# Kernel optimization log

Hardware: AMD Instinct MI355X
Metric: run time of the kernel (lower is better)

The kernel has to match this reference:

```python
import jax, jax.numpy as jnp
import numpy as np

D = 256; H = 8; L = 4; K = 4; AS = 2; HD = D // H
KK = K * K
LEVEL_SHAPES = [(128, 128), (64, 64), (32, 32), (16, 16)]


def _kernel_indices():
    # kernel_size=4 (even): linspace(-1.5, 1.5, 4); stack [j, i] then / K
    idx = jnp.linspace(-1.5, 1.5, K)
    ii, jj = jnp.meshgrid(idx, idx, indexing='ij')
    return jnp.stack([jj, ii], axis=-1).reshape(-1, 2) / K  # (KK, 2)


def _bilinear(vf, g, Hl, Wl):
    # vf: (b, H, Hl*Wl, HD) per-level value; g: (b, l1, H, KK, 2) in [0,1]
    # grid_sample semantics, align_corners=False, zero padding
    b, l1, h, kk, _ = g.shape
    x = g[..., 0] * Wl - 0.5
    y = g[..., 1] * Hl - 0.5
    x0 = jnp.floor(x)
    y0 = jnp.floor(y)
    acc = None
    for dx, dy in ((0, 0), (1, 0), (0, 1), (1, 1)):
        xi = x0 + dx
        yi = y0 + dy
        w = (1.0 - jnp.abs(x - xi)) * (1.0 - jnp.abs(y - yi))
        valid = (xi >= 0) & (xi < Wl) & (yi >= 0) & (yi < Hl)
        idx = (jnp.clip(yi, 0, Hl - 1) * Wl + jnp.clip(xi, 0, Wl - 1)).astype(jnp.int32)
        idx = idx.transpose(0, 2, 1, 3).reshape(b, h, l1 * kk)
        gth = jnp.take_along_axis(vf, idx[..., None], axis=2)  # (b,H,l1*kk,HD)
        ww = (w * valid).transpose(0, 2, 1, 3).reshape(b, h, l1 * kk)
        c = gth * ww[..., None]
        acc = c if acc is None else acc + c
    return acc.reshape(b, h, l1, kk, HD).transpose(0, 2, 1, 3, 4)  # (b,l1,H,kk,HD)


def setup_inputs() -> dict:
    key = jax.random.key(0)
    ks = jax.random.split(key, 9)
    b, l1 = 4, 1024
    l2 = sum(h * w for h, w in LEVEL_SHAPES)  # 21760
    query = jax.random.normal(ks[0], (b, l1, D), jnp.float32)
    value = jax.random.normal(ks[1], (b, l2, D), jnp.float32)
    centers = jax.random.uniform(ks[2], (b, l1, 2), jnp.float32)
    sizes = jax.random.uniform(ks[3], (b, l1, 2), jnp.float32) * 0.2 + 0.05
    ref_windows = jnp.concatenate([centers, sizes], axis=-1)  # (b,l1,4) cx,cy,w,h
    s = 1.0 / np.sqrt(D)
    Wv = jax.random.normal(ks[4], (D, D), jnp.float32) * s
    bv = jnp.zeros((D,), jnp.float32)
    Wo = jax.random.normal(ks[5], (D, D), jnp.float32) * s
    bo = jnp.zeros((D,), jnp.float32)
    Wbox = jax.random.normal(ks[6], (L * H * 4, D), jnp.float32) * 0.01
    bbox = jax.random.uniform(ks[7], (H * L * 4,), jnp.float32)
    Wattn = jax.random.normal(ks[8], (H * L * AS * AS, D), jnp.float32) * s
    battn = jnp.zeros((H * L * AS * AS,), jnp.float32)
    v_shape = np.array(LEVEL_SHAPES, np.int64)
    starts = np.cumsum([0] + [h * w for h, w in LEVEL_SHAPES[:-1]])
    v_start_index = np.array(starts, np.int64)
    v_mask = jnp.zeros((b, l2), bool)
    return dict(query=query, value=value, ref_windows=ref_windows, Wv=Wv, bv=bv,
                Wo=Wo, bo=bo, Wbox=Wbox, bbox=bbox, Wattn=Wattn, battn=battn,
                v_shape=v_shape, v_start_index=v_start_index, v_mask=v_mask)


def reference(query, value, ref_windows, Wv, bv, Wo, bo, Wbox, bbox, Wattn, battn,
              v_shape, v_start_index, v_mask):
    b, l1, _ = query.shape
    l2 = value.shape[1]
    # value projection + padding mask
    v = value @ Wv.T + bv
    v = jnp.where(v_mask[..., None], 0.0, v).reshape(b, l2, H, HD)
    # where to attend: offset boxes -> sampling grid (normalizer=None branch)
    off = (query @ Wbox.T + bbox).reshape(b, l1, H, L, 4)
    refw = ref_windows[:, :, None, None, :]            # (b,l1,1,1,4)
    refsz = jnp.concatenate([refw[..., 2:4], refw[..., 2:4]], axis=-1)
    boxes = refw + off / 8.0 * refsz                   # (b,l1,H,L,4)
    center = boxes[..., None, :2]
    size = boxes[..., None, 2:]
    grid = center + _kernel_indices() * jax.nn.relu(size)  # (b,l1,H,L,KK,2)
    # attention weights (attn_size grid upsampled to kernel_size by repeat_interleave)
    aw = (query @ Wattn.T + battn).reshape(b, l1, H, L, AS, AS)
    nr = K // AS
    aw = jnp.repeat(jnp.repeat(aw, nr, axis=-1), nr, axis=-2)  # (b,l1,H,L,K,K)
    sw = jax.nn.softmax(aw.reshape(b, l1, H, -1), axis=-1).reshape(b, l1, H, L, KK)
    lw = jax.nn.softmax(aw, axis=3).reshape(b, l1, H, L, KK)
    out = jnp.zeros((b, l1, H, HD), query.dtype)
    mout = jnp.zeros((b, l1, H, HD), query.dtype)
    for li in range(L):
        Hl, Wl = int(v_shape[li, 0]), int(v_shape[li, 1])
        st = int(v_start_index[li])
        vf = v[:, st:st + Hl * Wl].transpose(0, 2, 1, 3)  # (b,H,Hl*Wl,HD)
        samp = _bilinear(vf, grid[:, :, :, li], Hl, Wl)   # (b,l1,H,KK,HD)
        out = out + jnp.einsum('bqhkd,bqhk->bqhd', samp, sw[:, :, :, li])
        mout = mout + jnp.einsum('bqhkd,bqhk->bqhd', samp, lw[:, :, :, li])
    out = out.reshape(b, l1, D) @ Wo.T + bo
    mout = mout.reshape(b, l1, D) @ Wo.T + bo
    return out, mout, aw
```

## Files before the change

### kernel.cpp

```cpp
#include <hip/hip_runtime.h>
#include <hip/hip_bf16.h>


typedef __attribute__((ext_vector_type(8))) short short8;
typedef __attribute__((ext_vector_type(4))) float f32x4;

__device__ __forceinline__ unsigned short f2bf(float f) {
    unsigned int u = __float_as_uint(f);
    unsigned int r = u + 0x7FFFu + ((u >> 16) & 1u);
    return (unsigned short)(r >> 16);
}
__device__ __forceinline__ float bf2f(unsigned short s) {
    return __uint_as_float(((unsigned int)s) << 16);
}
__device__ __forceinline__ short8 pack2(float4 x, float4 y) {
    short8 r;
    r[0] = (short)f2bf(x.x); r[1] = (short)f2bf(x.y);
    r[2] = (short)f2bf(x.z); r[3] = (short)f2bf(x.w);
    r[4] = (short)f2bf(y.x); r[5] = (short)f2bf(y.y);
    r[6] = (short)f2bf(y.z); r[7] = (short)f2bf(y.w);
    return r;
}

__device__ __forceinline__ void storeC(float* C, size_t i, float v) { C[i] = v; }
__device__ __forceinline__ void storeC(unsigned short* C, size_t i, float v) { C[i] = f2bf(v); }

#define LDA 56

template <typename OutT>
__device__ __forceinline__ void gemm_body(
    const float* __restrict__ A, const float* __restrict__ W,
    const float* __restrict__ bias, OutT* __restrict__ C,
    int N, int bm, int bn)
{
    __shared__ __align__(16) unsigned short As[128 * LDA];
    __shared__ __align__(16) unsigned short Ws[128 * LDA];
    const int tid  = threadIdx.x;
    const int lane = tid & 63;
    const int wave = tid >> 6;
    const int wm = (wave & 1) * 64;
    const int wn = (wave >> 1) * 64;
    const int lr = tid >> 1;
    const int lh = (tid & 1) * 16;
    const int kg = lane >> 4;
    const int lm = lane & 15;

    f32x4 acc[4][4];
#pragma unroll
    for (int i = 0; i < 4; ++i)
#pragma unroll
        for (int j = 0; j < 4; ++j) {
            acc[i][j][0] = 0.f; acc[i][j][1] = 0.f;
            acc[i][j][2] = 0.f; acc[i][j][3] = 0.f;
        }

    const float* Ap = A + (size_t)(bm + lr) * 256 + lh;
    const float* Wp = W + (size_t)(bn + lr) * 256 + lh;
    unsigned short* Asp = &As[lr * LDA + lh];
    unsigned short* Wsp = &Ws[lr * LDA + lh];

    for (int k0 = 0; k0 < 256; k0 += 32) {
        float4 a0 = *(const float4*)(Ap + k0);
        float4 a1 = *(const float4*)(Ap + k0 + 4);
        float4 a2 = *(const float4*)(Ap + k0 + 8);
        float4 a3 = *(const float4*)(Ap + k0 + 12);
        float4 w0 = *(const float4*)(Wp + k0);
        float4 w1 = *(const float4*)(Wp + k0 + 4);
        float4 w2 = *(const float4*)(Wp + k0 + 8);
        float4 w3 = *(const float4*)(Wp + k0 + 12);
        __syncthreads();
        *(short8*)(Asp)     = pack2(a0, a1);
        *(short8*)(Asp + 8) = pack2(a2, a3);
        *(short8*)(Wsp)     = pack2(w0, w1);
        *(short8*)(Wsp + 8) = pack2(w2, w3);
        __syncthreads();
        short8 af[4], bfr[4];
#pragma unroll
        for (int i = 0; i < 4; ++i)
            af[i] = *(const short8*)&As[(wm + i * 16 + lm) * LDA + kg * 8];
#pragma unroll
        for (int j = 0; j < 4; ++j)
            bfr[j] = *(const short8*)&Ws[(wn + j * 16 + lm) * LDA + kg * 8];
#pragma unroll
        for (int i = 0; i < 4; ++i)
#pragma unroll
            for (int j = 0; j < 4; ++j)
                acc[i][j] = __builtin_amdgcn_mfma_f32_16x16x32_bf16(
                    af[i], bfr[j], acc[i][j], 0, 0, 0);
    }

#pragma unroll
    for (int j = 0; j < 4; ++j) {
        int col = bn + wn + j * 16 + lm;
        float bcol = bias[col];
#pragma unroll
        for (int i = 0; i < 4; ++i) {
#pragma unroll
            for (int r = 0; r < 4; ++r) {
                int row = bm + wm + i * 16 + kg * 4 + r;
                storeC(C, (size_t)row * N + col, acc[i][j][r] + bcol);
            }
        }
    }
}

__global__ __launch_bounds__(256) void gemm_v_kernel(
    const float* __restrict__ A, const float* __restrict__ W,
    const float* __restrict__ bias, unsigned short* __restrict__ C)
{
    gemm_body<unsigned short>(A, W, bias, C, 256, blockIdx.x * 128, blockIdx.y * 128);
}

__global__ __launch_bounds__(256) void gemm_f_kernel(
    const float* __restrict__ A, const float* __restrict__ W,
    const float* __restrict__ bias, float* __restrict__ C, int N)
{
    gemm_body<float>(A, W, bias, C, N, blockIdx.x * 128, blockIdx.y * 128);
}

__global__ __launch_bounds__(256) void gemm_qdual_kernel(
    const float* __restrict__ A,
    const float* __restrict__ W0, const float* __restrict__ b0, float* __restrict__ C0,
    const float* __restrict__ W1, const float* __restrict__ b1, float* __restrict__ C1)
{
    const float* W = blockIdx.y ? W1 : W0;
    const float* bb = blockIdx.y ? b1 : b0;
    float* C = blockIdx.y ? C1 : C0;
    gemm_body<float>(A, W, bb, C, 128, blockIdx.x * 128, 0);
}

__global__ __launch_bounds__(256) void sample_kernel(
    const unsigned short* __restrict__ v, const float* __restrict__ off,
    const float* __restrict__ awr, const float* __restrict__ refw,
    float* __restrict__ aw_out, float* __restrict__ acc)
{
    const int bq = blockIdx.x;
    const int b  = bq >> 10;
    const int t  = threadIdx.x;

    __shared__ float ref4[4];
    __shared__ float awl[128];
    __shared__ float bxs[128];
    __shared__ float swl[512];
    __shared__ float lwl[512];
    __shared__ int   sidx[512][4];
    __shared__ float swo[512][4];
    __shared__ float swm[512][4];

    if (t < 4)   ref4[t] = refw[bq * 4 + t];
    if (t < 128) awl[t] = awr[(size_t)bq * 128 + t];
    __syncthreads();

    if (t < 128) {
        float o = off[(size_t)bq * 128 + t];
        int comp = t & 3;
        float r0 = ref4[0], r1 = ref4[1], r2 = ref4[2], r3 = ref4[3];
        float bx;
        if (comp == 0)      bx = r0 + o * 0.125f * r2;
        else if (comp == 1) bx = r1 + o * 0.125f * r3;
        else if (comp == 2) bx = r2 + o * 0.125f * r2;
        else                bx = r3 + o * 0.125f * r3;
        bxs[t] = bx;

        const int h = t >> 4, r = t & 15;
        float a = awl[t];
        float m = a;
#pragma unroll
        for (int s = 1; s < 16; s <<= 1) m = fmaxf(m, __shfl_xor(m, s, 16));
        float se = expf(a - m);
#pragma unroll
        for (int s = 1; s < 16; s <<= 1) se += __shfl_xor(se, s, 16);
        const float inv_s = 1.0f / (4.0f * se);

        float* awq = aw_out + (size_t)bq * 512 + h * 64;
#pragma unroll
        for (int j = 0; j < 4; ++j) {
            int eidx = r * 4 + j;
            int l  = eidx >> 4;
            int ky = (eidx >> 2) & 3;
            int kx = eidx & 3;
            int pos = (ky >> 1) * 2 + (kx >> 1);
            float raw = awl[h * 16 + l * 4 + pos];
            swl[h * 64 + eidx] = expf(raw - m) * inv_s;
            int base = h * 16 + pos;
            float m2 = awl[base];
#pragma unroll
            for (int li = 1; li < 4; ++li) m2 = fmaxf(m2, awl[base + li * 4]);
            float s2 = 0.f;
#pragma unroll
            for (int li = 0; li < 4; ++li) s2 += expf(awl[base + li * 4] - m2);
            lwl[h * 64 + eidx] = expf(raw - m2) / s2;
            awq[eidx] = raw;
        }
    }
    __syncthreads();

    const int STs_[4] = {0, 16384, 20480, 21504};
    for (int e = t; e < 512; e += 256) {
        int eh = e >> 6, rem = e & 63, l = rem >> 4, kk = rem & 15;
        const float* bx = &bxs[eh * 16 + l * 4];
        float cx = bx[0], cy = bx[1];
        float bw = fmaxf(bx[2], 0.f), bh = fmaxf(bx[3], 0.f);
        float kx = -0.375f + 0.25f * (float)(kk & 3);
        float ky = -0.375f + 0.25f * (float)(kk >> 2);
        int Wl = 128 >> l;
        float x = (cx + kx * bw) * (float)Wl - 0.5f;
        float y = (cy + ky * bh) * (float)Wl - 0.5f;
        float x0f = floorf(x), y0f = floorf(y);
        int x0 = (int)x0f, y0 = (int)y0f;
        float fx = x - x0f, fy = y - y0f;
        float sww = swl[e], lww = lwl[e];
        int rowbase = b * 21760 + STs_[l];
#pragma unroll
        for (int tap = 0; tap < 4; ++tap) {
            int dx = tap & 1, dy = tap >> 1;
            int xi = x0 + dx, yi = y0 + dy;
            float w = (dx ? fx : 1.f - fx) * (dy ? fy : 1.f - fy);
            if (xi < 0 || xi >= Wl || yi < 0 || yi >= Wl) w = 0.f;
            int xc = min(max(xi, 0), Wl - 1);
            int yc = min(max(yi, 0), Wl - 1);
            sidx[e][tap] = (rowbase + yc * Wl + xc) << 8;
            swo[e][tap] = w * sww;
            swm[e][tap] = w * lww;
        }
    }
    __syncthreads();

    const int h = t >> 5;
    float ao = 0.f, am = 0.f;
#pragma unroll 4
    for (int i = 0; i < 64; ++i) {
        int e = h * 64 + i;
#pragma unroll
        for (int tap = 0; tap < 4; ++tap) {
            float val = bf2f(v[(size_t)(sidx[e][tap] + t)]);
            ao = fmaf(val, swo[e][tap], ao);
            am = fmaf(val, swm[e][tap], am);
        }
    }
    acc[(size_t)bq * 256 + t]          = ao;
    acc[(size_t)(4096 + bq) * 256 + t] = am;
}

extern "C" void kernel_launch(void* const* d_in, const int* in_sizes, int n_in,
                              void* d_out, int out_size, void* d_ws, size_t ws_size,
                              hipStream_t stream) {
    const float* query = (const float*)d_in[0];
    const float* value = (const float*)d_in[1];
    const float* refw  = (const float*)d_in[2];
    const float* Wv    = (const float*)d_in[3];
    const float* bv    = (const float*)d_in[4];
    const float* Wo    = (const float*)d_in[5];
    const float* bo    = (const float*)d_in[6];
    const float* Wbox  = (const float*)d_in[7];
    const float* bbox  = (const float*)d_in[8];
    const float* Wattn = (const float*)d_in[9];
    const float* battn = (const float*)d_in[10];

    float* out = (float*)d_out;
    float* aw_out = out + 2 * 1048576;

    unsigned short* v = (unsigned short*)d_ws;
    float* off = (float*)((char*)d_ws + 44564480);
    float* awr = off + 524288;
    float* acc = awr + 524288;

    gemm_v_kernel<<<dim3(680, 2), 256, 0, stream>>>(value, Wv, bv, v);
    gemm_qdual_kernel<<<dim3(32, 2), 256, 0, stream>>>(query, Wbox, bbox, off,
                                                       Wattn, battn, awr);
    sample_kernel<<<4096, 256, 0, stream>>>(v, off, awr, refw, aw_out, acc);
    gemm_f_kernel<<<dim3(64, 2), 256, 0, stream>>>(acc, Wo, bo, out, 256);
}
```

Measured before the change: 281.2 us.

## Merge value/query GEMMs, pack tap tables, gather bf16 pairs in sampler

The value-projection GEMM and the two query GEMMs now run in one launch, which removes a kernel launch and lets the small query blocks fill the tail of the large one. The sampling kernel packs each tap's index and two weights into one int4 in a padded shared table. Each thread now gathers two bf16 channels at once with a 32-bit load, and the two half-waves split the taps and combine their sums with a shuffle. It also remaps blocks so neighbouring blocks cover different batches, uses the packed bf16 conversion intrinsic, and adds more instructions for the shuffle reduction.

```diff
diff --git a/kernel.cpp b/kernel.cpp
--- a/kernel.cpp
+++ b/kernel.cpp
@@ -4,22 +4,22 @@
 
 typedef __attribute__((ext_vector_type(8))) short short8;
 typedef __attribute__((ext_vector_type(4))) float f32x4;
+typedef __attribute__((ext_vector_type(4))) unsigned int uint4v;
 
 __device__ __forceinline__ unsigned short f2bf(float f) {
     unsigned int u = __float_as_uint(f);
     unsigned int r = u + 0x7FFFu + ((u >> 16) & 1u);
     return (unsigned short)(r >> 16);
 }
-__device__ __forceinline__ float bf2f(unsigned short s) {
-    return __uint_as_float(((unsigned int)s) << 16);
+__device__ __forceinline__ unsigned int pkbf(float a, float b) {
+    __hip_bfloat162 h = __float22bfloat162_rn(float2{a, b});
+    return *reinterpret_cast<unsigned int*>(&h);
 }
 __device__ __forceinline__ short8 pack2(float4 x, float4 y) {
-    short8 r;
-    r[0] = (short)f2bf(x.x); r[1] = (short)f2bf(x.y);
-    r[2] = (short)f2bf(x.z); r[3] = (short)f2bf(x.w);
-    r[4] = (short)f2bf(y.x); r[5] = (short)f2bf(y.y);
-    r[6] = (short)f2bf(y.z); r[7] = (short)f2bf(y.w);
-    return r;
+    uint4v u;
+    u[0] = pkbf(x.x, x.y); u[1] = pkbf(x.z, x.w);
+    u[2] = pkbf(y.x, y.y); u[3] = pkbf(y.z, y.w);
+    return __builtin_bit_cast(short8, u);
 }
 
 __device__ __forceinline__ void storeC(float* C, size_t i, float v) { C[i] = v; }
@@ -31,10 +31,8 @@
 __device__ __forceinline__ void gemm_body(
     const float* __restrict__ A, const float* __restrict__ W,
     const float* __restrict__ bias, OutT* __restrict__ C,
-    int N, int bm, int bn)
-{
-    __shared__ __align__(16) unsigned short As[128 * LDA];
-    __shared__ __align__(16) unsigned short Ws[128 * LDA];
+    int N, int bm, int bn, unsigned short* As, unsigned short* Ws)
+{
     const int tid  = threadIdx.x;
     const int lane = tid & 63;
     const int wave = tid >> 6;
@@ -104,29 +102,34 @@
     }
 }
 
-__global__ __launch_bounds__(256) void gemm_v_kernel(
-    const float* __restrict__ A, const float* __restrict__ W,
-    const float* __restrict__ bias, unsigned short* __restrict__ C)
-{
-    gemm_body<unsigned short>(A, W, bias, C, 256, blockIdx.x * 128, blockIdx.y * 128);
+__global__ __launch_bounds__(256) void gemm_vq_kernel(
+    const float* __restrict__ value, const float* __restrict__ Wv,
+    const float* __restrict__ bv, unsigned short* __restrict__ v,
+    const float* __restrict__ query,
+    const float* __restrict__ Wbox, const float* __restrict__ bbox, float* __restrict__ off,
+    const float* __restrict__ Wattn, const float* __restrict__ battn, float* __restrict__ awr)
+{
+    __shared__ __align__(16) unsigned short As[128 * LDA];
+    __shared__ __align__(16) unsigned short Ws[128 * LDA];
+    const int x = blockIdx.x;
+    if (x < 1360) {
+        gemm_body<unsigned short>(value, Wv, bv, v, 256,
+                                  (x >> 1) * 128, (x & 1) * 128, As, Ws);
+    } else {
+        const int idx = x - 1360;
+        const int bm = (idx & 31) * 128;
+        if (idx < 32) gemm_body<float>(query, Wbox, bbox, off, 128, bm, 0, As, Ws);
+        else          gemm_body<float>(query, Wattn, battn, awr, 128, bm, 0, As, Ws);
+    }
 }
 
 __global__ __launch_bounds__(256) void gemm_f_kernel(
     const float* __restrict__ A, const float* __restrict__ W,
     const float* __restrict__ bias, float* __restrict__ C, int N)
 {
-    gemm_body<float>(A, W, bias, C, N, blockIdx.x * 128, blockIdx.y * 128);
-}
-
-__global__ __launch_bounds__(256) void gemm_qdual_kernel(
-    const float* __restrict__ A,
-    const float* __restrict__ W0, const float* __restrict__ b0, float* __restrict__ C0,
-    const float* __restrict__ W1, const float* __restrict__ b1, float* __restrict__ C1)
-{
-    const float* W = blockIdx.y ? W1 : W0;
-    const float* bb = blockIdx.y ? b1 : b0;
-    float* C = blockIdx.y ? C1 : C0;
-    gemm_body<float>(A, W, bb, C, 128, blockIdx.x * 128, 0);
+    __shared__ __align__(16) unsigned short As[128 * LDA];
+    __shared__ __align__(16) unsigned short Ws[128 * LDA];
+    gemm_body<float>(A, W, bias, C, N, blockIdx.x * 128, blockIdx.y * 128, As, Ws);
 }
 
 __global__ __launch_bounds__(256) void sample_kernel(
@@ -134,7 +137,8 @@
     const float* __restrict__ awr, const float* __restrict__ refw,
     float* __restrict__ aw_out, float* __restrict__ acc)
 {
-    const int bq = blockIdx.x;
+    const int x  = blockIdx.x;
+    const int bq = ((x & 3) << 10) | (x >> 2);
     const int b  = bq >> 10;
     const int t  = threadIdx.x;
 
@@ -143,9 +147,7 @@
     __shared__ float bxs[128];
     __shared__ float swl[512];
     __shared__ float lwl[512];
-    __shared__ int   sidx[512][4];
-    __shared__ float swo[512][4];
-    __shared__ float swm[512][4];
+    __shared__ int4  tp[16 * 129];
 
     if (t < 4)   ref4[t] = refw[bq * 4 + t];
     if (t < 128) awl[t] = awr[(size_t)bq * 128 + t];
@@ -204,13 +206,15 @@
         float kx = -0.375f + 0.25f * (float)(kk & 3);
         float ky = -0.375f + 0.25f * (float)(kk >> 2);
         int Wl = 128 >> l;
-        float x = (cx + kx * bw) * (float)Wl - 0.5f;
-        float y = (cy + ky * bh) * (float)Wl - 0.5f;
-        float x0f = floorf(x), y0f = floorf(y);
+        float xg = (cx + kx * bw) * (float)Wl - 0.5f;
+        float yg = (cy + ky * bh) * (float)Wl - 0.5f;
+        float x0f = floorf(xg), y0f = floorf(yg);
         int x0 = (int)x0f, y0 = (int)y0f;
-        float fx = x - x0f, fy = y - y0f;
+        float fx = xg - x0f, fy = yg - y0f;
         float sww = swl[e], lww = lwl[e];
         int rowbase = b * 21760 + STs_[l];
+        int seg = e >> 5;
+        int4* dst = &tp[seg * 129 + (e & 31) * 4];
 #pragma unroll
         for (int tap = 0; tap < 4; ++tap) {
             int dx = tap & 1, dy = tap >> 1;
@@ -219,27 +223,38 @@
             if (xi < 0 || xi >= Wl || yi < 0 || yi >= Wl) w = 0.f;
             int xc = min(max(xi, 0), Wl - 1);
             int yc = min(max(yi, 0), Wl - 1);
-            sidx[e][tap] = (rowbase + yc * Wl + xc) << 8;
-            swo[e][tap] = w * sww;
-            swm[e][tap] = w * lww;
+            dst[tap] = int4{(rowbase + yc * Wl + xc) << 7,
+                            __float_as_int(w * sww),
+                            __float_as_int(w * lww), 0};
         }
     }
     __syncthreads();
 
     const int h = t >> 5;
-    float ao = 0.f, am = 0.f;
+    const int half = (t >> 4) & 1;
+    const int c2 = t & 15;
+    const unsigned int* v32 = (const unsigned int*)v;
+    const int choff = h * 16 + c2;
+    const int4* tps = &tp[(h * 2 + half) * 129];
+
+    float ao0 = 0.f, ao1 = 0.f, am0 = 0.f, am1 = 0.f;
 #pragma unroll 4
-    for (int i = 0; i < 64; ++i) {
-        int e = h * 64 + i;
-#pragma unroll
-        for (int tap = 0; tap < 4; ++tap) {
-            float val = bf2f(v[(size_t)(sidx[e][tap] + t)]);
-            ao = fmaf(val, swo[e][tap], ao);
-            am = fmaf(val, swm[e][tap], am);
-        }
-    }
-    acc[(size_t)bq * 256 + t]          = ao;
-    acc[(size_t)(4096 + bq) * 256 + t] = am;
+    for (int i = 0; i < 128; ++i) {
+        int4 d = tps[i];
+        unsigned int pv = v32[(size_t)(d.x + choff)];
+        float v0 = __uint_as_float(pv << 16);
+        float v1 = __uint_as_float(pv & 0xffff0000u);
+        float wo = __int_as_float(d.y), wm = __int_as_float(d.z);
+        ao0 = fmaf(v0, wo, ao0); ao1 = fmaf(v1, wo, ao1);
+        am0 = fmaf(v0, wm, am0); am1 = fmaf(v1, wm, am1);
+    }
+    ao0 += __shfl_xor(ao0, 16); ao1 += __shfl_xor(ao1, 16);
+    am0 += __shfl_xor(am0, 16); am1 += __shfl_xor(am1, 16);
+    if (!half) {
+        size_t base = (size_t)bq * 256 + h * 32 + 2 * c2;
+        *(float2*)&acc[base]                       = float2{ao0, ao1};
+        *(float2*)&acc[base + (size_t)4096 * 256]  = float2{am0, am1};
+    }
 }
 
 extern "C" void kernel_launch(void* const* d_in, const int* in_sizes, int n_in,
@@ -265,9 +280,9 @@
     float* awr = off + 524288;
     float* acc = awr + 524288;
 
-    gemm_v_kernel<<<dim3(680, 2), 256, 0, stream>>>(value, Wv, bv, v);
-    gemm_qdual_kernel<<<dim3(32, 2), 256, 0, stream>>>(query, Wbox, bbox, off,
-                                                       Wattn, battn, awr);
+    gemm_vq_kernel<<<1424, 256, 0, stream>>>(value, Wv, bv, v,
+                                             query, Wbox, bbox, off,
+                                             Wattn, battn, awr);
     sample_kernel<<<4096, 256, 0, stream>>>(v, off, awr, refw, aw_out, acc);
     gemm_f_kernel<<<dim3(64, 2), 256, 0, stream>>>(acc, Wo, bo, out, 256);
 }
```

After: 275.8 us. Within noise of the previous version (-1.9%).
